# Kernel optimization log

Measured on AMD Instinct MI355X. Metric: run time of the kernel, lower is better.

## Reference

```python
import jax, jax.numpy as jnp
import numpy as np

B, NQ, NP_, D = 4, 2048, 8192, 256
T, H = 10, 4  # num_tables, num_hash_functions -> hash code length T*H = 40


def setup_inputs() -> dict:
    key = jax.random.key(0)
    k1, k2, k3 = jax.random.split(key, 3)
    return {
        "query_points": jax.random.normal(k1, (B, NQ, D), dtype=jnp.float32),
        "points": jax.random.normal(k2, (B, NP_, D), dtype=jnp.float32),
        "proj": jax.random.normal(k3, (T * H, D), dtype=jnp.float32),  # projection_matrices
        "k": 16,
    }


def _hash(x, proj):
    # x: [B, N, D], proj: [T*H, D] -> binary hash [B, N, T*H]
    return (jnp.einsum('bnd,fd->bnf', x, proj) > 0).astype(jnp.float32)


def reference(query_points, points, proj, k):
    qh = _hash(query_points, proj)   # [B, Nq, F]
    ph = _hash(points, proj)         # [B, Np, F]
    # L1 cdist on {0,1}-valued vectors == Hamming: |a-b| = a + b - 2ab (exact in fp32).
    sq = qh.sum(-1)                  # [B, Nq]
    sp = ph.sum(-1)                  # [B, Np]
    dist = sq[:, :, None] + sp[:, None, :] - 2.0 * jnp.einsum('bqf,bpf->bqp', qh, ph)
    kk = min(int(k), points.shape[1])
    neg_vals, indices = jax.lax.top_k(-dist, kk)  # smallest-k distances
    return indices, -neg_vals
```

## Files before the change

kernel.cpp:

```cpp
#include <hip/hip_runtime.h>
#include <stdint.h>

#define B_  4
#define NQ_ 2048
#define NP_ 8192
#define D_  256
#define F_  40
#define K_  16

__global__ __launch_bounds__(256) void hash_kernel(
    const float* __restrict__ qp, const float* __restrict__ pp,
    const float* __restrict__ proj, uint64_t* __restrict__ qcodes,
    uint64_t* __restrict__ pcodes) {
  __shared__ float tile[64 * 257];
  int t = threadIdx.x;
  int v0 = blockIdx.x * 64;
  bool isQ = v0 < B_ * NQ_;
  const float* src =
      isQ ? (qp + (size_t)v0 * D_) : (pp + (size_t)(v0 - B_ * NQ_) * D_);

#pragma unroll 8
  for (int i = 0; i < 64; ++i) tile[i * 257 + t] = src[i * 256 + t];
  __syncthreads();

  int lane = t & 63, w = t >> 6;
  int fbase = __builtin_amdgcn_readfirstlane(w * 10);
  const float* pj = proj + (size_t)fbase * 256;

  float acc[10];
#pragma unroll
  for (int f = 0; f < 10; ++f) acc[f] = 0.0f;
#pragma unroll 4
  for (int d = 0; d < 256; ++d) {
    float x = tile[lane * 257 + d];
#pragma unroll
    for (int f = 0; f < 10; ++f) acc[f] = fmaf(x, pj[f * 256 + d], acc[f]);
  }
  unsigned bits = 0;
#pragma unroll
  for (int f = 0; f < 10; ++f)
    if (acc[f] > 0.0f) bits |= 1u << f;

  __syncthreads();
  unsigned short* cb = (unsigned short*)tile;
  cb[lane * 4 + w] = (unsigned short)bits;
  __syncthreads();
  if (w == 0) {
    uint64_t code = (uint64_t)cb[lane * 4 + 0] |
                    ((uint64_t)cb[lane * 4 + 1] << 10) |
                    ((uint64_t)cb[lane * 4 + 2] << 20) |
                    ((uint64_t)cb[lane * 4 + 3] << 30);
    int gv = v0 + lane;
    if (isQ) qcodes[gv] = code;
    else pcodes[gv - B_ * NQ_] = code;
  }
}

__global__ __launch_bounds__(1024) void select_kernel(
    const uint64_t* __restrict__ qcodes, const uint64_t* __restrict__ pcodes,
    float* __restrict__ outIdx, float* __restrict__ outDist) {
  __shared__ ulonglong2 ldsP2[NP_ / 2];
  __shared__ unsigned keybuf[16][K_];
  uint64_t* ldsP = (uint64_t*)ldsP2;

  int tid = threadIdx.x;
  int bb = blockIdx.x >> 7;
  const uint64_t* pb = pcodes + (size_t)bb * NP_;
  for (int i = tid; i < NP_; i += 1024) ldsP[i] = pb[i];
  __syncthreads();

  int w = tid >> 6, lane = tid & 63;
  int qg = blockIdx.x * 16 + w;
  uint64_t qc = qcodes[qg];
  const uint64_t M = 0x00FF00FF00FF00FFull;

  uint64_t c8 = 0;
#pragma unroll 4
  for (int j = 0; j < 64; ++j) {
    ulonglong2 pc = ldsP2[j * 64 + lane];
    int d0 = __popcll(qc ^ pc.x);
    int d1 = __popcll(qc ^ pc.y);
    c8 += (1ull << (d0 & 56)) + (1ull << (d1 & 56));
  }
  uint64_t e = c8 & M, o = (c8 >> 8) & M;
#pragma unroll
  for (int s = 1; s < 64; s <<= 1) { e += __shfl_xor(e, s); o += __shfl_xor(o, s); }
  int Bb = 0; unsigned nbefore = 0, cum = 0; bool found = false;
#pragma unroll
  for (int k2 = 0; k2 < 6; ++k2) {
    unsigned c = (unsigned)(((k2 & 1) ? o : e) >> ((k2 >> 1) * 16)) & 0xFFFFu;
    if (!found && cum + c >= K_) { Bb = k2; nbefore = cum; found = true; }
    cum += c;
  }

  int base = Bb * 8;
  uint64_t cf = 0;
#pragma unroll 4
  for (int j = 0; j < 64; ++j) {
    ulonglong2 pc = ldsP2[j * 64 + lane];
    unsigned r0 = (unsigned)(__popcll(qc ^ pc.x) - base);
    unsigned r1 = (unsigned)(__popcll(qc ^ pc.y) - base);
    if (r0 < 8u) cf += 1ull << (r0 << 3);
    if (r1 < 8u) cf += 1ull << (r1 << 3);
  }
  e = cf & M; o = (cf >> 8) & M;
#pragma unroll
  for (int s = 1; s < 64; s <<= 1) { e += __shfl_xor(e, s); o += __shfl_xor(o, s); }
  int t = 0; unsigned n_lt = 0; cum = nbefore; found = false;
#pragma unroll
  for (int r = 0; r < 8; ++r) {
    unsigned c = (unsigned)(((r & 1) ? o : e) >> ((r >> 1) * 16)) & 0xFFFFu;
    if (!found && cum + c >= K_) { t = base + r; n_lt = cum; found = true; }
    cum += c;
  }
  unsigned r_need = K_ - n_lt;

  unsigned cl = 0, ce = 0;
  uint64_t lmask = (1ull << lane) - 1;
  for (int j = 0; j < 128; ++j) {
    int p = j * 64 + lane;
    int d = __popcll(qc ^ ldsP[p]);
    if (__any(d <= t)) {
      bool blt = (d < t), beq = (d == t);
      uint64_t mlt = __ballot(blt), meq = __ballot(beq);
      if (blt)
        keybuf[w][cl + (unsigned)__popcll(mlt & lmask)] =
            ((unsigned)d << 13) | (unsigned)p;
      if (beq) {
        unsigned pos = ce + (unsigned)__popcll(meq & lmask);
        if (pos < r_need)
          keybuf[w][n_lt + pos] = ((unsigned)d << 13) | (unsigned)p;
      }
      cl += (unsigned)__popcll(mlt);
      ce += (unsigned)__popcll(meq);
    }
  }
  __syncthreads();

  if (lane < K_) {
    unsigned my = keybuf[w][lane];
    int rank = 0;
#pragma unroll
    for (int jj = 0; jj < K_; ++jj) rank += (keybuf[w][jj] < my) ? 1 : 0;
    int off = qg * K_ + rank;
    outIdx[off]  = (float)(my & 8191u);
    outDist[off] = (float)(my >> 13);
  }
}

extern "C" void kernel_launch(void* const* d_in, const int* in_sizes, int n_in,
                              void* d_out, int out_size, void* d_ws, size_t ws_size,
                              hipStream_t stream) {
  const float* qp   = (const float*)d_in[0];
  const float* pp   = (const float*)d_in[1];
  const float* proj = (const float*)d_in[2];

  uint64_t* pcodes = (uint64_t*)d_ws;
  uint64_t* qcodes = pcodes + (size_t)B_ * NP_;

  float* outIdx  = (float*)d_out;
  float* outDist = outIdx + (size_t)B_ * NQ_ * K_;

  int total_vecs = B_ * (NQ_ + NP_);
  hash_kernel<<<total_vecs / 64, 256, 0, stream>>>(qp, pp, proj, qcodes, pcodes);
  select_kernel<<<B_ * NQ_ / 16, 1024, 0, stream>>>(qcodes, pcodes, outIdx, outDist);
}
```

Measured before the change: 172.8 us.

## Cache per-lane Hamming distances in registers and chunk hash tile loads

The select kernel now computes each of the 128 Hamming distances per lane once, packs them as bytes into 32 registers, and reuses them for the second histogram pass and the final collection pass. This replaces two further rounds of LDS reads and popcounts. The hash kernel loads its input tile in two 128-column halves, shrinking shared memory, and reads 8 values per step to batch FMAs. The cost is higher register pressure in the 1024-thread select kernel, which could spill, and an extra barrier pair in the hash kernel.

```diff
diff --git a/kernel.cpp b/kernel.cpp
--- a/kernel.cpp
+++ b/kernel.cpp
@@ -12,16 +12,12 @@
     const float* __restrict__ qp, const float* __restrict__ pp,
     const float* __restrict__ proj, uint64_t* __restrict__ qcodes,
     uint64_t* __restrict__ pcodes) {
-  __shared__ float tile[64 * 257];
+  __shared__ float tile[64 * 129];
   int t = threadIdx.x;
   int v0 = blockIdx.x * 64;
   bool isQ = v0 < B_ * NQ_;
   const float* src =
       isQ ? (qp + (size_t)v0 * D_) : (pp + (size_t)(v0 - B_ * NQ_) * D_);
-
-#pragma unroll 8
-  for (int i = 0; i < 64; ++i) tile[i * 257 + t] = src[i * 256 + t];
-  __syncthreads();
 
   int lane = t & 63, w = t >> 6;
   int fbase = __builtin_amdgcn_readfirstlane(w * 10);
@@ -30,11 +26,31 @@
   float acc[10];
 #pragma unroll
   for (int f = 0; f < 10; ++f) acc[f] = 0.0f;
-#pragma unroll 4
-  for (int d = 0; d < 256; ++d) {
-    float x = tile[lane * 257 + d];
+
+  int srow = t >> 7, scol = t & 127;
 #pragma unroll
-    for (int f = 0; f < 10; ++f) acc[f] = fmaf(x, pj[f * 256 + d], acc[f]);
+  for (int chunk = 0; chunk < 2; ++chunk) {
+    int doff = chunk * 128;
+    __syncthreads();
+#pragma unroll 8
+    for (int i = 0; i < 32; ++i) {
+      int row = i * 2 + srow;
+      tile[row * 129 + scol] = src[row * 256 + doff + scol];
+    }
+    __syncthreads();
+#pragma unroll
+    for (int dc = 0; dc < 128; dc += 8) {
+      float x8[8];
+#pragma unroll
+      for (int u = 0; u < 8; ++u) x8[u] = tile[lane * 129 + dc + u];
+      const float* prow = pj + doff + dc;
+#pragma unroll
+      for (int f = 0; f < 10; ++f) {
+#pragma unroll
+        for (int u = 0; u < 8; ++u)
+          acc[f] = fmaf(x8[u], prow[f * 256 + u], acc[f]);
+      }
+    }
   }
   unsigned bits = 0;
 #pragma unroll
@@ -59,9 +75,8 @@
 __global__ __launch_bounds__(1024) void select_kernel(
     const uint64_t* __restrict__ qcodes, const uint64_t* __restrict__ pcodes,
     float* __restrict__ outIdx, float* __restrict__ outDist) {
-  __shared__ ulonglong2 ldsP2[NP_ / 2];
+  __shared__ uint64_t ldsP[NP_];
   __shared__ unsigned keybuf[16][K_];
-  uint64_t* ldsP = (uint64_t*)ldsP2;
 
   int tid = threadIdx.x;
   int bb = blockIdx.x >> 7;
@@ -74,13 +89,20 @@
   uint64_t qc = qcodes[qg];
   const uint64_t M = 0x00FF00FF00FF00FFull;
 
+  unsigned dpack[32];
   uint64_t c8 = 0;
-#pragma unroll 4
-  for (int j = 0; j < 64; ++j) {
-    ulonglong2 pc = ldsP2[j * 64 + lane];
-    int d0 = __popcll(qc ^ pc.x);
-    int d1 = __popcll(qc ^ pc.y);
-    c8 += (1ull << (d0 & 56)) + (1ull << (d1 & 56));
+#pragma unroll
+  for (int jw = 0; jw < 32; ++jw) {
+    unsigned b0, b1, b2, b3;
+#pragma unroll
+    for (int s = 0; s < 4; ++s) {
+      uint64_t pc = ldsP[(jw * 4 + s) * 64 + lane];
+      unsigned d = (unsigned)__popcll(qc ^ pc);
+      c8 += 1ull << (d & 56);
+      if (s == 0) b0 = d; else if (s == 1) b1 = d;
+      else if (s == 2) b2 = d; else b3 = d;
+    }
+    dpack[jw] = b0 | (b1 << 8) | (b2 << 16) | (b3 << 24);
   }
   uint64_t e = c8 & M, o = (c8 >> 8) & M;
 #pragma unroll
@@ -93,46 +115,52 @@
     cum += c;
   }
 
-  int base = Bb * 8;
+  unsigned base = (unsigned)(Bb * 8);
   uint64_t cf = 0;
-#pragma unroll 4
-  for (int j = 0; j < 64; ++j) {
-    ulonglong2 pc = ldsP2[j * 64 + lane];
-    unsigned r0 = (unsigned)(__popcll(qc ^ pc.x) - base);
-    unsigned r1 = (unsigned)(__popcll(qc ^ pc.y) - base);
-    if (r0 < 8u) cf += 1ull << (r0 << 3);
-    if (r1 < 8u) cf += 1ull << (r1 << 3);
+#pragma unroll
+  for (int jw = 0; jw < 32; ++jw) {
+    unsigned word = dpack[jw];
+#pragma unroll
+    for (int s = 0; s < 4; ++s) {
+      unsigned rel = ((word >> (s * 8)) & 0xFFu) - base;
+      if (rel < 8u) cf += 1ull << (rel << 3);
+    }
   }
   e = cf & M; o = (cf >> 8) & M;
 #pragma unroll
   for (int s = 1; s < 64; s <<= 1) { e += __shfl_xor(e, s); o += __shfl_xor(o, s); }
-  int t = 0; unsigned n_lt = 0; cum = nbefore; found = false;
+  int thr = 0; unsigned n_lt = 0; cum = nbefore; found = false;
 #pragma unroll
   for (int r = 0; r < 8; ++r) {
     unsigned c = (unsigned)(((r & 1) ? o : e) >> ((r >> 1) * 16)) & 0xFFFFu;
-    if (!found && cum + c >= K_) { t = base + r; n_lt = cum; found = true; }
+    if (!found && cum + c >= K_) { thr = (int)(base + r); n_lt = cum; found = true; }
     cum += c;
   }
   unsigned r_need = K_ - n_lt;
 
   unsigned cl = 0, ce = 0;
   uint64_t lmask = (1ull << lane) - 1;
-  for (int j = 0; j < 128; ++j) {
-    int p = j * 64 + lane;
-    int d = __popcll(qc ^ ldsP[p]);
-    if (__any(d <= t)) {
-      bool blt = (d < t), beq = (d == t);
-      uint64_t mlt = __ballot(blt), meq = __ballot(beq);
-      if (blt)
-        keybuf[w][cl + (unsigned)__popcll(mlt & lmask)] =
-            ((unsigned)d << 13) | (unsigned)p;
-      if (beq) {
-        unsigned pos = ce + (unsigned)__popcll(meq & lmask);
-        if (pos < r_need)
-          keybuf[w][n_lt + pos] = ((unsigned)d << 13) | (unsigned)p;
+#pragma unroll
+  for (int jw = 0; jw < 32; ++jw) {
+    unsigned word = dpack[jw];
+#pragma unroll
+    for (int s = 0; s < 4; ++s) {
+      int d = (int)((word >> (s * 8)) & 0xFFu);
+      uint64_t mlt = __ballot(d < thr);
+      uint64_t meq = __ballot(d == thr);
+      if (mlt | meq) {
+        int p = (jw * 4 + s) * 64 + lane;
+        if (d < thr)
+          keybuf[w][cl + (unsigned)__popcll(mlt & lmask)] =
+              ((unsigned)d << 13) | (unsigned)p;
+        if (d == thr) {
+          unsigned pos = ce + (unsigned)__popcll(meq & lmask);
+          if (pos < r_need)
+            keybuf[w][n_lt + pos] = ((unsigned)d << 13) | (unsigned)p;
+        }
+        cl += (unsigned)__popcll(mlt);
+        ce += (unsigned)__popcll(meq);
       }
-      cl += (unsigned)__popcll(mlt);
-      ce += (unsigned)__popcll(meq);
     }
   }
   __syncthreads();
```

Result: slower. 288.6 us (+67.1%).
